# Kernel optimization log

Hardware: AMD Instinct MI355X
Metric: run time of the kernel (lower is better)

The kernel has to match this reference:

```python
import jax, jax.numpy as jnp
import numpy as np


def _attention(q, k, v, causal):
    # q,k,v: (B, S, H, D) -> matches flash_attn_func input layout
    B, Sq, H, D = q.shape
    Sk = k.shape[1]
    scale = 1.0 / jnp.sqrt(jnp.asarray(D, dtype=q.dtype))
    # scores: (B, H, Sq, Sk)
    scores = jnp.einsum('bqhd,bkhd->bhqk', q, k) * scale
    if causal:
        # position i attends to j <= i (standard causal mask, Sq == Sk here)
        mask = jnp.tril(jnp.ones((Sq, Sk), dtype=bool))
        scores = jnp.where(mask[None, None], scores, jnp.asarray(-jnp.inf, dtype=scores.dtype))
    probs = jax.nn.softmax(scores, axis=-1)
    out = jnp.einsum('bhqk,bkhd->bqhd', probs, v)
    return out


def setup_inputs() -> dict:
    key = jax.random.key(0)
    kq, kk, kv = jax.random.split(key, 3)
    B, S, H, D = 2, 2048, 16, 128
    q = jax.random.normal(kq, (B, S, H, D), dtype=jnp.float32)
    k = jax.random.normal(kk, (B, S, H, D), dtype=jnp.float32)
    v = jax.random.normal(kv, (B, S, H, D), dtype=jnp.float32)
    return {"q": q, "k": k, "v": v, "causal": 1}


def reference(q, k, v, causal):
    return _attention(q, k, v, bool(causal))
```

## Files before the change

### kernel.cpp

```cpp
#include <hip/hip_runtime.h>

typedef short bf16x8 __attribute__((ext_vector_type(8)));
typedef float f32x16 __attribute__((ext_vector_type(16)));

constexpr int S = 2048;
constexpr int H = 16;
constexpr int D = 128;
constexpr int BM = 128;
constexpr int TILE = 8192;
constexpr int KSTR = 136;


__device__ inline unsigned int pk2(float a, float b) {
    unsigned int ua = __builtin_bit_cast(unsigned int, a);
    unsigned int ub = __builtin_bit_cast(unsigned int, b);
    ua += 0x7fffu + ((ua >> 16) & 1u);
    ub += 0x7fffu + ((ub >> 16) & 1u);
    return (ua >> 16) | (ub & 0xffff0000u);
}

__device__ __forceinline__ void gld16(const unsigned short* g, unsigned short* l) {
    __builtin_amdgcn_global_load_lds(
        (const __attribute__((address_space(1))) unsigned int*)g,
        (__attribute__((address_space(3))) unsigned int*)l, 16, 0, 0);
}

__global__ __launch_bounds__(256) void cvt_kv(const float* __restrict__ K,
                                              const float* __restrict__ V,
                                              unsigned short* __restrict__ Kb,
                                              unsigned short* __restrict__ Vtb) {
    __shared__ unsigned short Vl[64 * KSTR];
    const int tid = threadIdx.x;
    const int t   = blockIdx.x;
    const int bh  = blockIdx.y;
    const int b = bh >> 4, h = bh & 15;
    const size_t base = ((size_t)(b * S + t * 64) * H + h) * D;

    unsigned short* outK = Kb + ((size_t)bh * 32 + t) * TILE;
    #pragma unroll
    for (int u = 0; u < 4; ++u) {
        const int dlin = u * 256 + tid;
        const int grp = dlin >> 7;
        const int s   = dlin & 127;
        const int rho = s >> 4;
        const int c   = (s & 15) ^ rho;
        const float* p = K + base + (size_t)(grp * 8 + rho) * (H * D) + c * 8;
        float4 f0 = *(const float4*)p;
        float4 f1 = *(const float4*)(p + 4);
        unsigned int w[4];
        w[0] = pk2(f0.x, f0.y); w[1] = pk2(f0.z, f0.w);
        w[2] = pk2(f1.x, f1.y); w[3] = pk2(f1.z, f1.w);
        *(uint4*)(outK + dlin * 8) = *(const uint4*)w;
    }

    #pragma unroll
    for (int u = 0; u < 4; ++u) {
        const int cidx = tid + 256 * u;
        const int n    = cidx >> 4;
        const int off  = (cidx & 15) * 8;
        const float* p = V + base + (size_t)n * (H * D) + off;
        float4 f0 = *(const float4*)p;
        float4 f1 = *(const float4*)(p + 4);
        unsigned int w[4];
        w[0] = pk2(f0.x, f0.y); w[1] = pk2(f0.z, f0.w);
        w[2] = pk2(f1.x, f1.y); w[3] = pk2(f1.z, f1.w);
        *(uint4*)&Vl[n * KSTR + off] = *(const uint4*)w;
    }
    __syncthreads();

    const int d  = tid >> 1;
    const int kh = (tid & 1) * 32;
    unsigned short tmp[32];
    #pragma unroll
    for (int m = 0; m < 32; ++m) {
        const int sig = kh + m;
        const int k = (sig & ~12) | ((sig & 4) << 1) | ((sig & 8) >> 1);
        tmp[m] = Vl[k * KSTR + d];
    }
    unsigned short* outV = Vtb + ((size_t)bh * 32 + t) * TILE;
    const int g = d >> 3, rho = d & 7;
    #pragma unroll
    for (int uu = 0; uu < 4; ++uu) {
        const int cc = (kh >> 3) + uu;
        *(uint4*)(outV + g * 512 + (rho * 8 + (cc ^ rho)) * 8) = *(const uint4*)&tmp[uu * 8];
    }
}

__global__ __launch_bounds__(256, 1) void fa_fwd(
    const float* __restrict__ Q,
    const unsigned short* __restrict__ Kb,
    const unsigned short* __restrict__ Vtb,
    const int* __restrict__ causal_p,
    float* __restrict__ Op)
{
    __shared__ unsigned short Kl[3][TILE];
    __shared__ unsigned short Vl[3][TILE];

    const int tid  = threadIdx.x;
    const int wave = tid >> 6;
    const int lane = tid & 63;
    const int ln   = lane & 31;
    const int half = lane >> 5;

    int bh, qp;
    if (gridDim.x == 8 && gridDim.y == 32) {
        const int lid = blockIdx.x + (blockIdx.y << 3);
        const int xcd = lid & 7;
        const int ii  = lid >> 3;
        bh = (xcd << 2) + (ii & 3);
        qp = ii >> 2;
    } else {
        bh = blockIdx.y;
        qp = blockIdx.x;
    }
    const int b = bh >> 4;
    const int h = bh & 15;
    const int causal = *causal_p;
    const float cfold = 0.12751743f;

    const unsigned short* Ksrc = Kb  + (size_t)bh * (32 * TILE);
    const unsigned short* Vsrc = Vtb + (size_t)bh * (32 * TILE);
    const int sg   = wave * 4;
    const int loff = lane * 8;

    const int kb   = (ln >> 3) * 1024 + (ln & 7) * 128;
    const int krho = ln & 7;
    const int vg   = (ln >> 3) * 512;
    const int vrho = ln & 7;

    #pragma unroll 1
    for (int ph = 0; ph < 2; ++ph) {
        const int qblk  = ph ? (15 - qp) : qp;
        const int q0    = qblk * BM;
        const int qrow0 = q0 + wave * 32;
        const int jmax  = causal ? ((q0 + BM - 1) >> 6) : (S / 64 - 1);

        bf16x8 qf[8];
        {
            const size_t rowoff = ((size_t)(b * S + qrow0 + ln) * H + h) * D;
            #pragma unroll
            for (int c = 0; c < 8; ++c) {
                float4 f0 = *(const float4*)(Q + rowoff + c * 16 + half * 8);
                float4 f1 = *(const float4*)(Q + rowoff + c * 16 + half * 8 + 4);
                unsigned int t[4];
                t[0] = pk2(f0.x * cfold, f0.y * cfold);
                t[1] = pk2(f0.z * cfold, f0.w * cfold);
                t[2] = pk2(f1.x * cfold, f1.y * cfold);
                t[3] = pk2(f1.z * cfold, f1.w * cfold);
                qf[c] = *(const bf16x8*)t;
            }
        }

        #pragma unroll
        for (int qq = 0; qq < 4; ++qq) {
            gld16(Ksrc + (sg + qq) * 512 + loff, &Kl[0][(sg + qq) * 512]);
            gld16(Vsrc + (sg + qq) * 512 + loff, &Vl[0][(sg + qq) * 512]);
        }
        #pragma unroll
        for (int qq = 0; qq < 4; ++qq) {
            gld16(Ksrc + TILE + (sg + qq) * 512 + loff, &Kl[1][(sg + qq) * 512]);
            gld16(Vsrc + TILE + (sg + qq) * 512 + loff, &Vl[1][(sg + qq) * 512]);
        }
        asm volatile("s_waitcnt vmcnt(8)" ::: "memory");
        __builtin_amdgcn_s_barrier();

        f32x16 o[4];
        #pragma unroll
        for (int dt = 0; dt < 4; ++dt)
            #pragma unroll
            for (int r = 0; r < 16; ++r) o[dt][r] = 0.0f;
        float l = 0.0f;

        int cur = 0;
        #pragma unroll 1
        for (int j = 0; j <= jmax; ++j) {
            const bool pf2 = (j + 2 <= jmax);
            if (pf2) {
                int nxt = cur + 2; if (nxt >= 3) nxt -= 3;
                const unsigned short* ks = Ksrc + (size_t)(j + 2) * TILE;
                const unsigned short* vs = Vsrc + (size_t)(j + 2) * TILE;
                #pragma unroll
                for (int qq = 0; qq < 4; ++qq) {
                    gld16(ks + (sg + qq) * 512 + loff, &Kl[nxt][(sg + qq) * 512]);
                    gld16(vs + (sg + qq) * 512 + loff, &Vl[nxt][(sg + qq) * 512]);
                }
            }

            const bool active = (!causal) || (j * 64 <= qrow0 + 31);
            if (active) {
                const unsigned short* Klc = Kl[cur];
                const unsigned short* Vtc = Vl[cur];

                f32x16 sacc[2];
                #pragma unroll
                for (int nt = 0; nt < 2; ++nt) {
                    #pragma unroll
                    for (int r = 0; r < 16; ++r) sacc[nt][r] = 0.0f;
                    const unsigned short* kl = Klc + nt * 4096 + kb;
                    #pragma unroll
                    for (int c = 0; c < 8; ++c) {
                        uint4 raw = *(const uint4*)(kl + (((2 * c + half) ^ krho) << 3));
                        bf16x8 kf = *(const bf16x8*)&raw;
                        sacc[nt] = __builtin_amdgcn_mfma_f32_32x32x16_bf16(kf, qf[c], sacc[nt], 0, 0, 0);
                    }
                }

                float p[32];
                const int thr  = qrow0 + ln - j * 64;
                const bool full = (!causal) || (j * 64 + 63 <= qrow0);
                #pragma unroll
                for (int nt = 0; nt < 2; ++nt)
                    #pragma unroll
                    for (int r = 0; r < 16; ++r) {
                        float e = __builtin_amdgcn_exp2f(sacc[nt][r]);
                        if (!full) {
                            const int kl_ = nt * 32 + (r & 3) + 8 * (r >> 2) + 4 * half;
                            if (kl_ > thr) e = 0.0f;
                        }
                        l += e;
                        p[nt * 16 + r] = e;
                    }

                #pragma unroll
                for (int win = 0; win < 4; ++win) {
                    unsigned int pw[4];
                    #pragma unroll
                    for (int d2 = 0; d2 < 4; ++d2)
                        pw[d2] = pk2(p[win * 8 + 2 * d2], p[win * 8 + 2 * d2 + 1]);
                    bf16x8 pf = *(const bf16x8*)pw;
                    const int voff = ((vrho * 8) + ((win * 2 + half) ^ vrho)) << 3;
                    #pragma unroll
                    for (int dt = 0; dt < 4; ++dt) {
                        uint4 raw = *(const uint4*)(Vtc + dt * 2048 + vg + voff);
                        bf16x8 vf = *(const bf16x8*)&raw;
                        o[dt] = __builtin_amdgcn_mfma_f32_32x32x16_bf16(vf, pf, o[dt], 0, 0, 0);
                    }
                }
            }

            if (pf2) asm volatile("s_waitcnt vmcnt(8)" ::: "memory");
            else     asm volatile("s_waitcnt vmcnt(0)" ::: "memory");
            __builtin_amdgcn_s_barrier();
            cur += 1; if (cur >= 3) cur -= 3;
        }

        const float lt  = l + __shfl_xor(l, 32);
        const float inv = 1.0f / lt;
        float* op = Op + ((size_t)(b * S + qrow0 + ln) * H + h) * D;
        #pragma unroll
        for (int dt = 0; dt < 4; ++dt)
            #pragma unroll
            for (int rq = 0; rq < 4; ++rq) {
                float4 st;
                st.x = o[dt][rq * 4 + 0] * inv;
                st.y = o[dt][rq * 4 + 1] * inv;
                st.z = o[dt][rq * 4 + 2] * inv;
                st.w = o[dt][rq * 4 + 3] * inv;
                *(float4*)(op + dt * 32 + 8 * rq + 4 * half) = st;
            }
    }
}

extern "C" void kernel_launch(void* const* d_in, const int* in_sizes, int n_in,
                              void* d_out, int out_size, void* d_ws, size_t ws_size,
                              hipStream_t stream) {
    const int B = in_sizes[0] / (S * H * D);
    unsigned short* Kb  = (unsigned short*)d_ws;
    unsigned short* Vtb = Kb + (size_t)B * S * H * D;

    cvt_kv<<<dim3(S / 64, B * H), 256, 0, stream>>>(
        (const float*)d_in[1], (const float*)d_in[2], Kb, Vtb);
    fa_fwd<<<dim3(8, B * H), 256, 0, stream>>>(
        (const float*)d_in[0], Kb, Vtb, (const int*)d_in[3], (float*)d_out);
}
```

Baseline: 202.4 us.

## Split key tile across two wave groups with 512-thread blocks and LDS reduction

Doubles the block to 8 waves. Each pair of waves shares a 32-row query slice and handles half of each 64-key tile, and the partial outputs and row sums are combined through shared memory at the end. The K/V pipeline drops from triple to double buffering to free LDS for the reduction buffers, and s_setprio is wrapped around the MFMA sections. The goal is more in-flight waves and finer causal skipping per wave. The cost is a full vmcnt(0) wait on every iteration and extra LDS traffic and barriers in the epilogue.

```diff
diff --git a/kernel.cpp b/kernel.cpp
--- a/kernel.cpp
+++ b/kernel.cpp
@@ -86,21 +86,25 @@
     }
 }
 
-__global__ __launch_bounds__(256, 1) void fa_fwd(
+__global__ __launch_bounds__(512, 2) void fa_fwd(
     const float* __restrict__ Q,
     const unsigned short* __restrict__ Kb,
     const unsigned short* __restrict__ Vtb,
     const int* __restrict__ causal_p,
     float* __restrict__ Op)
 {
-    __shared__ unsigned short Kl[3][TILE];
-    __shared__ unsigned short Vl[3][TILE];
+    __shared__ unsigned short Kl[2][TILE];
+    __shared__ unsigned short Vl[2][TILE];
+    __shared__ float mbf[4][64 * 36];
+    __shared__ float lbf[4][32];
 
     const int tid  = threadIdx.x;
-    const int wave = tid >> 6;
+    const int w    = tid >> 6;
     const int lane = tid & 63;
     const int ln   = lane & 31;
     const int half = lane >> 5;
+    const int qw   = w & 3;
+    const int nt   = w >> 2;
 
     int bh, qp;
     if (gridDim.x == 8 && gridDim.y == 32) {
@@ -120,7 +124,7 @@
 
     const unsigned short* Ksrc = Kb  + (size_t)bh * (32 * TILE);
     const unsigned short* Vsrc = Vtb + (size_t)bh * (32 * TILE);
-    const int sg   = wave * 4;
+    const int sgk  = w * 2;
     const int loff = lane * 8;
 
     const int kb   = (ln >> 3) * 1024 + (ln & 7) * 128;
@@ -132,8 +136,14 @@
     for (int ph = 0; ph < 2; ++ph) {
         const int qblk  = ph ? (15 - qp) : qp;
         const int q0    = qblk * BM;
-        const int qrow0 = q0 + wave * 32;
+        const int qrow0 = q0 + qw * 32;
         const int jmax  = causal ? ((q0 + BM - 1) >> 6) : (S / 64 - 1);
+
+        #pragma unroll
+        for (int c2 = 0; c2 < 2; ++c2) {
+            gld16(Ksrc + (sgk + c2) * 512 + loff, &Kl[0][(sgk + c2) * 512]);
+            gld16(Vsrc + (sgk + c2) * 512 + loff, &Vl[0][(sgk + c2) * 512]);
+        }
 
         bf16x8 qf[8];
         {
@@ -151,19 +161,6 @@
             }
         }
 
-        #pragma unroll
-        for (int qq = 0; qq < 4; ++qq) {
-            gld16(Ksrc + (sg + qq) * 512 + loff, &Kl[0][(sg + qq) * 512]);
-            gld16(Vsrc + (sg + qq) * 512 + loff, &Vl[0][(sg + qq) * 512]);
-        }
-        #pragma unroll
-        for (int qq = 0; qq < 4; ++qq) {
-            gld16(Ksrc + TILE + (sg + qq) * 512 + loff, &Kl[1][(sg + qq) * 512]);
-            gld16(Vsrc + TILE + (sg + qq) * 512 + loff, &Vl[1][(sg + qq) * 512]);
-        }
-        asm volatile("s_waitcnt vmcnt(8)" ::: "memory");
-        __builtin_amdgcn_s_barrier();
-
         f32x16 o[4];
         #pragma unroll
         for (int dt = 0; dt < 4; ++dt)
@@ -171,93 +168,127 @@
             for (int r = 0; r < 16; ++r) o[dt][r] = 0.0f;
         float l = 0.0f;
 
+        asm volatile("s_waitcnt vmcnt(0)" ::: "memory");
+        __builtin_amdgcn_s_barrier();
+
         int cur = 0;
         #pragma unroll 1
         for (int j = 0; j <= jmax; ++j) {
-            const bool pf2 = (j + 2 <= jmax);
-            if (pf2) {
-                int nxt = cur + 2; if (nxt >= 3) nxt -= 3;
-                const unsigned short* ks = Ksrc + (size_t)(j + 2) * TILE;
-                const unsigned short* vs = Vsrc + (size_t)(j + 2) * TILE;
-                #pragma unroll
-                for (int qq = 0; qq < 4; ++qq) {
-                    gld16(ks + (sg + qq) * 512 + loff, &Kl[nxt][(sg + qq) * 512]);
-                    gld16(vs + (sg + qq) * 512 + loff, &Vl[nxt][(sg + qq) * 512]);
+            if (j < jmax) {
+                const unsigned short* ks = Ksrc + (size_t)(j + 1) * TILE;
+                const unsigned short* vs = Vsrc + (size_t)(j + 1) * TILE;
+                #pragma unroll
+                for (int c2 = 0; c2 < 2; ++c2) {
+                    gld16(ks + (sgk + c2) * 512 + loff, &Kl[cur ^ 1][(sgk + c2) * 512]);
+                    gld16(vs + (sgk + c2) * 512 + loff, &Vl[cur ^ 1][(sgk + c2) * 512]);
                 }
             }
 
-            const bool active = (!causal) || (j * 64 <= qrow0 + 31);
-            if (active) {
-                const unsigned short* Klc = Kl[cur];
-                const unsigned short* Vtc = Vl[cur];
-
-                f32x16 sacc[2];
-                #pragma unroll
-                for (int nt = 0; nt < 2; ++nt) {
-                    #pragma unroll
-                    for (int r = 0; r < 16; ++r) sacc[nt][r] = 0.0f;
-                    const unsigned short* kl = Klc + nt * 4096 + kb;
-                    #pragma unroll
-                    for (int c = 0; c < 8; ++c) {
-                        uint4 raw = *(const uint4*)(kl + (((2 * c + half) ^ krho) << 3));
-                        bf16x8 kf = *(const bf16x8*)&raw;
-                        sacc[nt] = __builtin_amdgcn_mfma_f32_32x32x16_bf16(kf, qf[c], sacc[nt], 0, 0, 0);
-                    }
-                }
-
-                float p[32];
+            const bool wact = (!causal) || (j * 64 + nt * 32 <= qrow0 + 31);
+            if (wact) {
+                f32x16 sacc;
+                #pragma unroll
+                for (int r = 0; r < 16; ++r) sacc[r] = 0.0f;
+                const unsigned short* kl = &Kl[cur][nt * 4096 + kb];
+                __builtin_amdgcn_s_setprio(1);
+                #pragma unroll
+                for (int c = 0; c < 8; ++c) {
+                    uint4 raw = *(const uint4*)(kl + (((2 * c + half) ^ krho) << 3));
+                    bf16x8 kf = *(const bf16x8*)&raw;
+                    sacc = __builtin_amdgcn_mfma_f32_32x32x16_bf16(kf, qf[c], sacc, 0, 0, 0);
+                }
+                __builtin_amdgcn_s_setprio(0);
+
+                float p[16];
                 const int thr  = qrow0 + ln - j * 64;
                 const bool full = (!causal) || (j * 64 + 63 <= qrow0);
                 #pragma unroll
-                for (int nt = 0; nt < 2; ++nt)
-                    #pragma unroll
-                    for (int r = 0; r < 16; ++r) {
-                        float e = __builtin_amdgcn_exp2f(sacc[nt][r]);
-                        if (!full) {
-                            const int kl_ = nt * 32 + (r & 3) + 8 * (r >> 2) + 4 * half;
-                            if (kl_ > thr) e = 0.0f;
-                        }
-                        l += e;
-                        p[nt * 16 + r] = e;
+                for (int r = 0; r < 16; ++r) {
+                    float e = __builtin_amdgcn_exp2f(sacc[r]);
+                    if (!full) {
+                        const int kl_ = nt * 32 + (r & 3) + 8 * (r >> 2) + 4 * half;
+                        if (kl_ > thr) e = 0.0f;
                     }
-
-                #pragma unroll
-                for (int win = 0; win < 4; ++win) {
+                    l += e;
+                    p[r] = e;
+                }
+
+                __builtin_amdgcn_s_setprio(1);
+                #pragma unroll
+                for (int win2 = 0; win2 < 2; ++win2) {
                     unsigned int pw[4];
                     #pragma unroll
                     for (int d2 = 0; d2 < 4; ++d2)
-                        pw[d2] = pk2(p[win * 8 + 2 * d2], p[win * 8 + 2 * d2 + 1]);
+                        pw[d2] = pk2(p[win2 * 8 + 2 * d2], p[win2 * 8 + 2 * d2 + 1]);
                     bf16x8 pf = *(const bf16x8*)pw;
-                    const int voff = ((vrho * 8) + ((win * 2 + half) ^ vrho)) << 3;
+                    const int cc = (nt * 2 + win2) * 2 + half;
+                    const int voff = ((vrho * 8) + (cc ^ vrho)) << 3;
                     #pragma unroll
                     for (int dt = 0; dt < 4; ++dt) {
-                        uint4 raw = *(const uint4*)(Vtc + dt * 2048 + vg + voff);
+                        uint4 raw = *(const uint4*)(&Vl[cur][dt * 2048 + vg + voff]);
                         bf16x8 vf = *(const bf16x8*)&raw;
                         o[dt] = __builtin_amdgcn_mfma_f32_32x32x16_bf16(vf, pf, o[dt], 0, 0, 0);
                     }
                 }
+                __builtin_amdgcn_s_setprio(0);
             }
 
-            if (pf2) asm volatile("s_waitcnt vmcnt(8)" ::: "memory");
-            else     asm volatile("s_waitcnt vmcnt(0)" ::: "memory");
+            asm volatile("s_waitcnt vmcnt(0)" ::: "memory");
             __builtin_amdgcn_s_barrier();
-            cur += 1; if (cur >= 3) cur -= 3;
-        }
-
-        const float lt  = l + __shfl_xor(l, 32);
-        const float inv = 1.0f / lt;
-        float* op = Op + ((size_t)(b * S + qrow0 + ln) * H + h) * D;
-        #pragma unroll
-        for (int dt = 0; dt < 4; ++dt)
-            #pragma unroll
-            for (int rq = 0; rq < 4; ++rq) {
-                float4 st;
-                st.x = o[dt][rq * 4 + 0] * inv;
-                st.y = o[dt][rq * 4 + 1] * inv;
-                st.z = o[dt][rq * 4 + 2] * inv;
-                st.w = o[dt][rq * 4 + 3] * inv;
-                *(float4*)(op + dt * 32 + 8 * rq + 4 * half) = st;
-            }
+            cur ^= 1;
+        }
+
+        const float lp = l + __shfl_xor(l, 32);
+        float* mb = mbf[qw];
+        if (w >= 4) {
+            #pragma unroll
+            for (int dt = 0; dt < 2; ++dt)
+                #pragma unroll
+                for (int r = 0; r < 16; ++r)
+                    mb[lane * 36 + dt * 16 + r] = o[dt][r];
+            if (half == 0) lbf[qw][ln] = lp;
+        }
+        __syncthreads();
+        float ltot = 1.0f;
+        if (w < 4) {
+            #pragma unroll
+            for (int dt = 0; dt < 2; ++dt)
+                #pragma unroll
+                for (int r = 0; r < 16; ++r)
+                    o[dt][r] += mb[lane * 36 + dt * 16 + r];
+            ltot = lp + lbf[qw][ln];
+        }
+        __syncthreads();
+        if (w >= 4) {
+            #pragma unroll
+            for (int dt = 2; dt < 4; ++dt)
+                #pragma unroll
+                for (int r = 0; r < 16; ++r)
+                    mb[lane * 36 + (dt - 2) * 16 + r] = o[dt][r];
+        }
+        __syncthreads();
+        if (w < 4) {
+            #pragma unroll
+            for (int dt = 2; dt < 4; ++dt)
+                #pragma unroll
+                for (int r = 0; r < 16; ++r)
+                    o[dt][r] += mb[lane * 36 + (dt - 2) * 16 + r];
+
+            const float inv = 1.0f / ltot;
+            float* op = Op + ((size_t)(b * S + qrow0 + ln) * H + h) * D;
+            #pragma unroll
+            for (int dt = 0; dt < 4; ++dt)
+                #pragma unroll
+                for (int rq = 0; rq < 4; ++rq) {
+                    float4 st;
+                    st.x = o[dt][rq * 4 + 0] * inv;
+                    st.y = o[dt][rq * 4 + 1] * inv;
+                    st.z = o[dt][rq * 4 + 2] * inv;
+                    st.w = o[dt][rq * 4 + 3] * inv;
+                    *(float4*)(op + dt * 32 + 8 * rq + 4 * half) = st;
+                }
+        }
+        __syncthreads();
     }
 }
 
@@ -270,6 +301,6 @@
 
     cvt_kv<<<dim3(S / 64, B * H), 256, 0, stream>>>(
         (const float*)d_in[1], (const float*)d_in[2], Kb, Vtb);
-    fa_fwd<<<dim3(8, B * H), 256, 0, stream>>>(
+    fa_fwd<<<dim3(8, B * H), 512, 0, stream>>>(
         (const float*)d_in[0], Kb, Vtb, (const int*)d_in[3], (float*)d_out);
 }
```

New measurement: 191.6 us. 1.06x faster.
